# Performance work log

Measured on AMD Instinct MI355X. Metric: run time of the kernel, lower is better.

## Reference

```python
import jax, jax.numpy as jnp
import numpy as np

# Model dims (match init_kwargs)
B, S, H = 1, 2048, 1024
E = 16            # n_routed_experts
I = 768           # moe_intermediate_size
TOPK = 4          # num_experts_per_tok
G = 4             # n_group
TOPK_G = 2        # topk_group
SCALE = 2.5       # routed_scaling_factor
N_SHARED = 1      # n_shared_experts


def setup_inputs() -> dict:
    key = jax.random.key(0)
    ks = jax.random.split(key, 9)
    def rn(k, shape, scale=0.02):
        return jax.random.normal(k, shape, dtype=jnp.float32) * scale
    return dict(
        hidden_states=jax.random.normal(ks[0], (B, S, H), dtype=jnp.float32),
        gate_w=rn(ks[1], (E, H)),
        gate_bias=jax.random.normal(ks[2], (E,), dtype=jnp.float32) * 0.1,
        w1=rn(ks[3], (E, I, H)),   # gate_proj weights [out,in]
        w2=rn(ks[4], (E, H, I)),   # down_proj weights
        w3=rn(ks[5], (E, I, H)),   # up_proj weights
        ws1=rn(ks[6], (I * N_SHARED, H)),
        ws2=rn(ks[7], (H, I * N_SHARED)),
        ws3=rn(ks[8], (I * N_SHARED, H)),
    )


def _route(x, gate_w, gate_bias):
    """noaux_tc routing: sigmoid scores + bias, group top-k, top_k experts."""
    n = x.shape[0]
    logits = jnp.einsum('nh,eh->ne', x.astype(jnp.float32), gate_w)  # [N,E]
    scores = jax.nn.sigmoid(logits)
    sb = scores + gate_bias                                          # biased scores
    # group score = sum of top-2 biased scores in each group
    gs = sb.reshape(n, G, E // G)
    group_scores = jnp.sum(jax.lax.top_k(gs, 2)[0], axis=-1)         # [N,G]
    _, gidx = jax.lax.top_k(group_scores, TOPK_G)                    # [N,TOPK_G]
    gmask = jnp.sum(jax.nn.one_hot(gidx, G, dtype=sb.dtype), axis=1) # [N,G]
    emask = jnp.repeat(gmask, E // G, axis=-1)                       # [N,E]
    masked = jnp.where(emask > 0, sb, -jnp.inf)
    _, tidx = jax.lax.top_k(masked, TOPK)                            # [N,TOPK]
    w = jnp.take_along_axis(scores, tidx, axis=1)                    # unbiased weights
    w = w / (jnp.sum(w, axis=-1, keepdims=True) + 1e-20)             # norm_topk_prob
    return tidx, w * SCALE


def reference(hidden_states, gate_w, gate_bias, w1, w2, w3, ws1, ws2, ws3):
    b, s, h = hidden_states.shape
    x = hidden_states.reshape(-1, h)                                 # [N,H]
    tidx, tw = _route(x, gate_w, gate_bias)
    n = x.shape[0]
    # dense combine weights [N,E] (zero for unselected experts)
    combine = jnp.zeros((n, E), x.dtype).at[jnp.arange(n)[:, None], tidx].add(tw)
    # grouped SwiGLU experts (dense-over-experts reference form)
    g = jnp.einsum('nh,eih->nei', x, w1)
    u = jnp.einsum('nh,eih->nei', x, w3)
    hact = jax.nn.silu(g) * u * combine[:, :, None]
    y = jnp.einsum('nei,ehi->nh', hact, w2)
    # shared expert SwiGLU
    shared = jnp.einsum('ni,hi->nh', jax.nn.silu(x @ ws1.T) * (x @ ws3.T), ws2)
    return (y + shared).reshape(b, s, h)
```

## Files before the change

### kernel.cpp

```cpp
#include <hip/hip_runtime.h>
#include <hip/hip_bf16.h>
#include <math.h>

#define N_TOK 2048
#define H_DIM 1024
#define N_EXP 16
#define I_DIM 768
#define TOPK 4
#define SCALE 2.5f

#define GU_SLOTS 256
#define DN_SLOTS 192
#define GU_TAB (8 * GU_SLOTS)
#define DN_TAB (8 * DN_SLOTS)
#define GU_NY (I_DIM / 64)
#define DN_NY (H_DIM / 128)
#define MAX_GRP 832

typedef __attribute__((ext_vector_type(8))) short bf16x8;
typedef __attribute__((ext_vector_type(4))) float f32x4;

#define OFF_COUNTS   0
#define OFF_OFFSETS  128
#define OFF_WGU      256
#define OFF_WDN      (OFF_WGU + GU_TAB*4)
#define OFF_TOKIDS   (OFF_WDN + DN_TAB*4)
#define OFF_TOKW     (OFF_TOKIDS + N_EXP*N_TOK*4)
#define OFF_XB       (OFF_TOKW + N_EXP*N_TOK*4)
#define OFF_HACT     (OFF_XB + (size_t)N_TOK*H_DIM*2)
#define OFF_GWT      (OFF_HACT + (size_t)N_TOK*(TOPK+1)*I_DIM*2)

__device__ __forceinline__ ushort f2bf(float f) {
    union { __hip_bfloat16 h; ushort u; } cv;
    cv.h = __float2bfloat16(f);
    return cv.u;
}
__device__ __forceinline__ unsigned pack2(float lo, float hi) {
    return (unsigned)f2bf(lo) | ((unsigned)f2bf(hi) << 16);
}
__device__ __forceinline__ void async_copy16(const void* g, void* l) {
    __builtin_amdgcn_global_load_lds(
        (const __attribute__((address_space(1))) unsigned int*)g,
        (__attribute__((address_space(3))) unsigned int*)l, 16, 0, 0);
}

__global__ void k_gwt(const float* __restrict__ gw, float* __restrict__ gwT) {
    int i = blockIdx.x * 256 + threadIdx.x;
    int k = i >> 4, e = i & 15;
    gwT[i] = gw[e * H_DIM + k];
}

__launch_bounds__(256)
__global__ void k_route(const float* __restrict__ x, const float* __restrict__ gwT,
                        const float* __restrict__ gb,
                        int* __restrict__ counts, int* __restrict__ tok_ids,
                        float* __restrict__ tok_w, ushort* __restrict__ xb) {
    __shared__ float lgs[4][N_EXP + 1];
    int tid = threadIdx.x;
    int wv = tid >> 6, lane = tid & 63;
    int e = lane & 15, ks = lane >> 4;
    int n = blockIdx.x * 4 + wv;

    const float* xr = x + (size_t)n * H_DIM + ks * 256;
    ushort* xbr = xb + (size_t)n * H_DIM + ks * 256;
    const float* wr = gwT + ks * 256 * N_EXP + e;
    float a0 = 0.f, a1 = 0.f, a2 = 0.f, a3 = 0.f;
#pragma unroll 8
    for (int k = 0; k < 256; k += 4) {
        float4 xv = *(const float4*)(xr + k);
        a0 += xv.x * wr[(k + 0) * N_EXP];
        a1 += xv.y * wr[(k + 1) * N_EXP];
        a2 += xv.z * wr[(k + 2) * N_EXP];
        a3 += xv.w * wr[(k + 3) * N_EXP];
        if (e == 0) {
            uint2 p;
            p.x = pack2(xv.x, xv.y);
            p.y = pack2(xv.z, xv.w);
            *(uint2*)(xbr + k) = p;
        }
    }
    float acc = (a0 + a1) + (a2 + a3);
    acc += __shfl_xor(acc, 16);
    acc += __shfl_xor(acc, 32);
    if (lane < 16) lgs[wv][lane] = acc;
    __syncthreads();

    if (tid < 4) {
        int n2 = blockIdx.x * 4 + tid;
        float sc[N_EXP], sb[N_EXP];
        for (int ee = 0; ee < N_EXP; ee++) {
            float l = lgs[tid][ee];
            sc[ee] = 1.f / (1.f + expf(-l));
            sb[ee] = sc[ee] + gb[ee];
        }
        float gsc[4];
        for (int g = 0; g < 4; g++) {
            float m1 = -1e30f, m2 = -1e30f;
            for (int j = 0; j < 4; j++) {
                float v = sb[4 * g + j];
                if (v > m1) { m2 = m1; m1 = v; }
                else if (v > m2) m2 = v;
            }
            gsc[g] = m1 + m2;
        }
        int g1 = 0;
        for (int g = 1; g < 4; g++) if (gsc[g] > gsc[g1]) g1 = g;
        int g2 = -1;
        for (int g = 0; g < 4; g++) {
            if (g == g1) continue;
            if (g2 < 0 || gsc[g] > gsc[g2]) g2 = g;
        }
        bool allowed[N_EXP];
        for (int ee = 0; ee < N_EXP; ee++) {
            int grp = ee >> 2;
            allowed[ee] = (grp == g1) || (grp == g2);
        }
        int chosen[TOPK];
        float wsum = 0.f;
        for (int k = 0; k < TOPK; k++) {
            int best = -1;
            for (int ee = 0; ee < N_EXP; ee++) {
                if (!allowed[ee]) continue;
                if (best < 0 || sb[ee] > sb[best]) best = ee;
            }
            chosen[k] = best;
            allowed[best] = false;
            wsum += sc[best];
        }
        float inv = SCALE / (wsum + 1e-20f);
        for (int k = 0; k < TOPK; k++) {
            int ee = chosen[k];
            int p = atomicAdd(&counts[ee], 1);
            tok_ids[ee * N_TOK + p] = n2;
            tok_w[ee * N_TOK + p] = sc[ee] * inv;
        }
    }
}

__global__ void k_scan(const int* __restrict__ counts, int* __restrict__ offsets,
                       int* __restrict__ wgu, int* __restrict__ wdn) {
    __shared__ int nmt_s[20], gpe_s[20];
    __shared__ int geb[20], deb[20];
    __shared__ int gmeta[MAX_GRP];
    __shared__ int gslot[MAX_GRP];
    __shared__ int ngu_s, ntot_s;
    int tid = threadIdx.x;
    for (int i = tid; i < GU_TAB; i += 256) wgu[i] = -1;
    for (int i = tid; i < DN_TAB; i += 256) wdn[i] = -1;
    if (tid < 17) {
        int c = (tid == 16) ? N_TOK : counts[tid];
        int nm = (c + 127) >> 7;
        nmt_s[tid] = nm;
        gpe_s[tid] = (nm + 3) >> 2;
    }
    __syncthreads();
    if (tid == 0) {
        int off = 0;
        for (int e = 0; e < N_EXP; e++) { offsets[e] = off; off += counts[e]; }
        offsets[N_EXP] = off;
        int g = 0, d = 0;
        for (int e = 0; e <= N_EXP; e++) {
            geb[e] = g; g += GU_NY * gpe_s[e];
            deb[e] = d; d += DN_NY * gpe_s[e];
        }
        geb[N_EXP + 1] = g; deb[N_EXP + 1] = d;
        ngu_s = g; ntot_s = g + d;
    }
    __syncthreads();
    int ngu = ngu_s, ntot = ntot_s;
    for (int g = tid; g < ntot; g += 256) {
        bool gu = g < ngu;
        int r = gu ? g : g - ngu;
        const int* eb = gu ? geb : deb;
        int e = 0;
        while (eb[e + 1] <= r) e++;
        int rem = r - eb[e];
        int gp = gpe_s[e];
        int y = rem / gp, mc = rem - y * gp;
        int m0t = mc * 4;
        int size = nmt_s[e] - m0t; if (size > 4) size = 4;
        gmeta[g] = e | (m0t << 5) | (y << 9) | (size << 24);
    }
    __syncthreads();
    if (tid < 8) {
        int s = 0;
        for (int g = tid; g < ngu; g += 8) { gslot[g] = s; s += (gmeta[g] >> 24); }
    } else if (tid < 16) {
        int c = tid - 8, s = 0;
        for (int g = ngu + c; g < ntot; g += 8) { gslot[g] = s; s += (gmeta[g] >> 24); }
    }
    __syncthreads();
    int k = tid & 3;
    for (int g = tid >> 2; g < ntot; g += 64) {
        int p = gmeta[g];
        int size = (p >> 24);
        if (k >= size) continue;
        int desc = (p & 0x1FFF) + (k << 5);
        bool gu = g < ngu;
        int r = gu ? g : g - ngu;
        int idx = (r & 7) + 8 * (gslot[g] + k);
        if (gu) wgu[idx] = desc; else wdn[idx] = desc;
    }
}

__launch_bounds__(256, 3)
__global__ void k_gateup(const ushort* __restrict__ xb, const float* __restrict__ w1,
                         const float* __restrict__ w3, const float* __restrict__ ws1,
                         const float* __restrict__ ws3, const int* __restrict__ counts,
                         const int* __restrict__ offsets, const int* __restrict__ wgu,
                         const int* __restrict__ tok_ids, const float* __restrict__ tok_w,
                         ushort* __restrict__ hact) {
    int desc = wgu[blockIdx.x];
    if (desc < 0) return;
    int e = desc & 31;
    int m0 = ((desc >> 5) & 15) * 128;
    int i0 = ((desc >> 9) & 15) * 64;
    int Me = (e == N_EXP) ? N_TOK : counts[e];
    const float* W1 = (e == N_EXP) ? ws1 : w1 + (size_t)e * I_DIM * H_DIM;
    const float* W3 = (e == N_EXP) ? ws3 : w3 + (size_t)e * I_DIM * H_DIM;
    int base = offsets[e];

    __shared__ ushort As[128][64];
    __shared__ ushort Bs[128][64];
    __shared__ float tws[128];

    int tid = threadIdx.x;
    int wv = tid >> 6, lane = tid & 63;
    int seg = lane & 7, rsub = lane >> 3;
    int gch = (seg ^ rsub) * 8;

    if (tid < 128) {
        int r = m0 + tid;
        tws[tid] = (e == N_EXP) ? 1.f : ((r < Me) ? tok_w[e * N_TOK + r] : 0.f);
    }

    const ushort* aptr[4];
#pragma unroll
    for (int j = 0; j < 4; j++) {
        int gr = m0 + wv * 32 + j * 8 + rsub;
        int tok = (e == N_EXP) ? gr : ((gr < Me) ? tok_ids[e * N_TOK + gr] : 0);
        aptr[j] = xb + (size_t)tok * H_DIM + gch;
    }
    const float* bptrf[4];
#pragma unroll
    for (int j = 0; j < 4; j++) {
        int r = wv * 32 + j * 8 + rsub;
        const float* W = (r < 64) ? (W1 + (size_t)(i0 + r) * H_DIM)
                                  : (W3 + (size_t)(i0 + r - 64) * H_DIM);
        bptrf[j] = W + gch;
    }

    int quad = lane >> 4, lr = lane & 15, rx = lr & 7;
    f32x4 acc[2][8] = {};

    const int NK = H_DIM / 64;
    float4 bv0[4], bv1[4];
#pragma unroll
    for (int j = 0; j < 4; j++) {
        bv0[j] = *(const float4*)(bptrf[j]);
        bv1[j] = *(const float4*)(bptrf[j] + 4);
    }
    for (int k = 0; k < NK; k++) {
        int off = k * 64;
#pragma unroll
        for (int j = 0; j < 4; j++) async_copy16(aptr[j] + off, &As[wv * 32 + j * 8][0]);
#pragma unroll
        for (int j = 0; j < 4; j++) {
            uint4 p;
            p.x = pack2(bv0[j].x, bv0[j].y);
            p.y = pack2(bv0[j].z, bv0[j].w);
            p.z = pack2(bv1[j].x, bv1[j].y);
            p.w = pack2(bv1[j].z, bv1[j].w);
            *(uint4*)&Bs[wv * 32 + j * 8 + rsub][seg * 8] = p;
        }
        if (k + 1 < NK) {
#pragma unroll
            for (int j = 0; j < 4; j++) {
                bv0[j] = *(const float4*)(bptrf[j] + off + 64);
                bv1[j] = *(const float4*)(bptrf[j] + off + 68);
            }
        }
        __syncthreads();
#pragma unroll
        for (int ks = 0; ks < 2; ks++) {
            int co = ((ks * 4 + quad) ^ rx) * 8;
            bf16x8 a0 = *(const bf16x8*)&As[wv * 32 + lr][co];
            bf16x8 a1 = *(const bf16x8*)&As[wv * 32 + 16 + lr][co];
#pragma unroll
            for (int ni = 0; ni < 8; ni++) {
                bf16x8 bf = *(const bf16x8*)&Bs[ni * 16 + lr][co];
                acc[0][ni] = __builtin_amdgcn_mfma_f32_16x16x32_bf16(a0, bf, acc[0][ni], 0, 0, 0);
                acc[1][ni] = __builtin_amdgcn_mfma_f32_16x16x32_bf16(a1, bf, acc[1][ni], 0, 0, 0);
            }
        }
        __syncthreads();
    }

#pragma unroll
    for (int mi = 0; mi < 2; mi++) {
#pragma unroll
        for (int ni = 0; ni < 4; ni++) {
            f32x4 g = acc[mi][ni];
            f32x4 u = acc[mi][ni + 4];
#pragma unroll
            for (int rg = 0; rg < 4; rg++) {
                int ml = wv * 32 + mi * 16 + quad * 4 + rg;
                int row = m0 + ml;
                if (row < Me) {
                    float gg = g[rg], uu = u[rg];
                    float act = (gg / (1.f + expf(-gg))) * uu * tws[ml];
                    hact[(size_t)(base + row) * I_DIM + i0 + ni * 16 + lr] = f2bf(act);
                }
            }
        }
    }
}

__launch_bounds__(256, 3)
__global__ void k_down(const ushort* __restrict__ hact, const float* __restrict__ w2,
                       const float* __restrict__ ws2, const int* __restrict__ counts,
                       const int* __restrict__ offsets, const int* __restrict__ wdn,
                       const int* __restrict__ tok_ids, float* __restrict__ out) {
    int desc = wdn[blockIdx.x];
    if (desc < 0) return;
    int e = desc & 31;
    int m0 = ((desc >> 5) & 15) * 128;
    int h0 = ((desc >> 9) & 15) * 128;
    int Me = (e == N_EXP) ? N_TOK : counts[e];
    const float* W2 = (e == N_EXP) ? ws2 : w2 + (size_t)e * H_DIM * I_DIM;
    int base = offsets[e];

    __shared__ ushort As[128][64];
    __shared__ ushort Bs[128][64];
    __shared__ int toks[128];

    int tid = threadIdx.x;
    int wv = tid >> 6, lane = tid & 63;
    int seg = lane & 7, rsub = lane >> 3;
    int gch = (seg ^ rsub) * 8;

    if (tid < 128) {
        int r = m0 + tid;
        toks[tid] = (e == N_EXP) ? r : ((r < Me) ? tok_ids[e * N_TOK + r] : 0);
    }

    const ushort* aptr[4];
#pragma unroll
    for (int j = 0; j < 4; j++) {
        int row = wv * 32 + j * 8 + rsub;
        aptr[j] = hact + (size_t)(base + m0 + row) * I_DIM + gch;
    }
    const float* bptrf[4];
#pragma unroll
    for (int j = 0; j < 4; j++) {
        int r = wv * 32 + j * 8 + rsub;
        bptrf[j] = W2 + (size_t)(h0 + r) * I_DIM + gch;
    }

    int quad = lane >> 4, lr = lane & 15, rx = lr & 7;
    f32x4 acc[2][8] = {};

    const int NK = I_DIM / 64;
    float4 bv0[4], bv1[4];
#pragma unroll
    for (int j = 0; j < 4; j++) {
        bv0[j] = *(const float4*)(bptrf[j]);
        bv1[j] = *(const float4*)(bptrf[j] + 4);
    }
    for (int k = 0; k < NK; k++) {
        int off = k * 64;
#pragma unroll
        for (int j = 0; j < 4; j++) async_copy16(aptr[j] + off, &As[wv * 32 + j * 8][0]);
#pragma unroll
        for (int j = 0; j < 4; j++) {
            uint4 p;
            p.x = pack2(bv0[j].x, bv0[j].y);
            p.y = pack2(bv0[j].z, bv0[j].w);
            p.z = pack2(bv1[j].x, bv1[j].y);
            p.w = pack2(bv1[j].z, bv1[j].w);
            *(uint4*)&Bs[wv * 32 + j * 8 + rsub][seg * 8] = p;
        }
        if (k + 1 < NK) {
#pragma unroll
            for (int j = 0; j < 4; j++) {
                bv0[j] = *(const float4*)(bptrf[j] + off + 64);
                bv1[j] = *(const float4*)(bptrf[j] + off + 68);
            }
        }
        __syncthreads();
#pragma unroll
        for (int ks = 0; ks < 2; ks++) {
            int co = ((ks * 4 + quad) ^ rx) * 8;
            bf16x8 a0 = *(const bf16x8*)&As[wv * 32 + lr][co];
            bf16x8 a1 = *(const bf16x8*)&As[wv * 32 + 16 + lr][co];
#pragma unroll
            for (int ni = 0; ni < 8; ni++) {
                bf16x8 bf = *(const bf16x8*)&Bs[ni * 16 + lr][co];
                acc[0][ni] = __builtin_amdgcn_mfma_f32_16x16x32_bf16(a0, bf, acc[0][ni], 0, 0, 0);
                acc[1][ni] = __builtin_amdgcn_mfma_f32_16x16x32_bf16(a1, bf, acc[1][ni], 0, 0, 0);
            }
        }
        __syncthreads();
    }

#pragma unroll
    for (int mi = 0; mi < 2; mi++) {
#pragma unroll
        for (int ni = 0; ni < 8; ni++) {
#pragma unroll
            for (int rg = 0; rg < 4; rg++) {
                int ml = wv * 32 + mi * 16 + quad * 4 + rg;
                int row = m0 + ml;
                if (row < Me) {
                    int tok = toks[ml];
                    atomicAdd(&out[(size_t)tok * H_DIM + h0 + ni * 16 + lr],
                              acc[mi][ni][rg]);
                }
            }
        }
    }
}

extern "C" void kernel_launch(void* const* d_in, const int* in_sizes, int n_in,
                              void* d_out, int out_size, void* d_ws, size_t ws_size,
                              hipStream_t stream) {
    const float* x   = (const float*)d_in[0];
    const float* gw  = (const float*)d_in[1];
    const float* gb  = (const float*)d_in[2];
    const float* w1  = (const float*)d_in[3];
    const float* w2  = (const float*)d_in[4];
    const float* w3  = (const float*)d_in[5];
    const float* ws1 = (const float*)d_in[6];
    const float* ws2 = (const float*)d_in[7];
    const float* ws3 = (const float*)d_in[8];
    float* out = (float*)d_out;

    char* wsb = (char*)d_ws;
    int* counts   = (int*)(wsb + OFF_COUNTS);
    int* offsets  = (int*)(wsb + OFF_OFFSETS);
    int* wgu      = (int*)(wsb + OFF_WGU);
    int* wdn      = (int*)(wsb + OFF_WDN);
    int* tok_ids  = (int*)(wsb + OFF_TOKIDS);
    float* tok_w  = (float*)(wsb + OFF_TOKW);
    ushort* xb    = (ushort*)(wsb + OFF_XB);
    ushort* hact  = (ushort*)(wsb + OFF_HACT);
    float* gwT    = (float*)(wsb + OFF_GWT);

    hipMemsetAsync(wsb, 0, 128, stream);
    hipMemsetAsync(d_out, 0, (size_t)out_size * 4, stream);

    k_gwt<<<N_EXP * H_DIM / 256, 256, 0, stream>>>(gw, gwT);
    k_route<<<N_TOK / 4, 256, 0, stream>>>(x, gwT, gb, counts, tok_ids, tok_w, xb);
    k_scan<<<1, 256, 0, stream>>>(counts, offsets, wgu, wdn);
    k_gateup<<<GU_TAB, 256, 0, stream>>>(xb, w1, w3, ws1, ws3, counts, offsets,
                                         wgu, tok_ids, tok_w, hact);
    k_down<<<DN_TAB, 256, 0, stream>>>(hact, w2, ws2, counts, offsets, wdn,
                                       tok_ids, out);
}
```

Measured before the change: 364.7 us.

## Replace atomic scatter in down projection with staged buffer and per-token reduce

The down-projection kernel now writes each expert's partial outputs to a dense per-slot temporary buffer instead of issuing fp32 atomicAdds into the output. Routing records an inverse map from each token's top-k choices to expert slots, and a new reduce kernel sums the shared-expert row and the four routed rows per token. The output memset is dropped. This removes atomic contention and scattered atomic traffic, at the cost of an extra kernel launch and roughly 40MB of temporary writes and reads.

```diff
diff --git a/kernel.cpp b/kernel.cpp
--- a/kernel.cpp
+++ b/kernel.cpp
@@ -26,9 +26,11 @@
 #define OFF_WDN      (OFF_WGU + GU_TAB*4)
 #define OFF_TOKIDS   (OFF_WDN + DN_TAB*4)
 #define OFF_TOKW     (OFF_TOKIDS + N_EXP*N_TOK*4)
-#define OFF_XB       (OFF_TOKW + N_EXP*N_TOK*4)
+#define OFF_INV      (OFF_TOKW + N_EXP*N_TOK*4)
+#define OFF_XB       (OFF_INV + N_TOK*TOPK*4)
 #define OFF_HACT     (OFF_XB + (size_t)N_TOK*H_DIM*2)
 #define OFF_GWT      (OFF_HACT + (size_t)N_TOK*(TOPK+1)*I_DIM*2)
+#define OFF_YTMP     (OFF_GWT + N_EXP*H_DIM*4)
 
 __device__ __forceinline__ ushort f2bf(float f) {
     union { __hip_bfloat16 h; ushort u; } cv;
@@ -54,7 +56,8 @@
 __global__ void k_route(const float* __restrict__ x, const float* __restrict__ gwT,
                         const float* __restrict__ gb,
                         int* __restrict__ counts, int* __restrict__ tok_ids,
-                        float* __restrict__ tok_w, ushort* __restrict__ xb) {
+                        float* __restrict__ tok_w, ushort* __restrict__ xb,
+                        int* __restrict__ inv) {
     __shared__ float lgs[4][N_EXP + 1];
     int tid = threadIdx.x;
     int wv = tid >> 6, lane = tid & 63;
@@ -127,12 +130,13 @@
             allowed[best] = false;
             wsum += sc[best];
         }
-        float inv = SCALE / (wsum + 1e-20f);
+        float inv_w = SCALE / (wsum + 1e-20f);
         for (int k = 0; k < TOPK; k++) {
             int ee = chosen[k];
             int p = atomicAdd(&counts[ee], 1);
             tok_ids[ee * N_TOK + p] = n2;
-            tok_w[ee * N_TOK + p] = sc[ee] * inv;
+            tok_w[ee * N_TOK + p] = sc[ee] * inv_w;
+            inv[n2 * TOPK + k] = (ee << 16) | p;
         }
     }
 }
@@ -320,7 +324,7 @@
 __global__ void k_down(const ushort* __restrict__ hact, const float* __restrict__ w2,
                        const float* __restrict__ ws2, const int* __restrict__ counts,
                        const int* __restrict__ offsets, const int* __restrict__ wdn,
-                       const int* __restrict__ tok_ids, float* __restrict__ out) {
+                       float* __restrict__ ytmp) {
     int desc = wdn[blockIdx.x];
     if (desc < 0) return;
     int e = desc & 31;
@@ -332,17 +336,11 @@
 
     __shared__ ushort As[128][64];
     __shared__ ushort Bs[128][64];
-    __shared__ int toks[128];
 
     int tid = threadIdx.x;
     int wv = tid >> 6, lane = tid & 63;
     int seg = lane & 7, rsub = lane >> 3;
     int gch = (seg ^ rsub) * 8;
-
-    if (tid < 128) {
-        int r = m0 + tid;
-        toks[tid] = (e == N_EXP) ? r : ((r < Me) ? tok_ids[e * N_TOK + r] : 0);
-    }
 
     const ushort* aptr[4];
 #pragma unroll
@@ -412,13 +410,28 @@
                 int ml = wv * 32 + mi * 16 + quad * 4 + rg;
                 int row = m0 + ml;
                 if (row < Me) {
-                    int tok = toks[ml];
-                    atomicAdd(&out[(size_t)tok * H_DIM + h0 + ni * 16 + lr],
-                              acc[mi][ni][rg]);
+                    ytmp[(size_t)(base + row) * H_DIM + h0 + ni * 16 + lr] =
+                        acc[mi][ni][rg];
                 }
             }
         }
     }
+}
+
+__launch_bounds__(256)
+__global__ void k_reduce(const float* __restrict__ ytmp, const int* __restrict__ inv,
+                         const int* __restrict__ offsets, float* __restrict__ out) {
+    int t = blockIdx.x, tid = threadIdx.x;
+    const float4* yt = (const float4*)ytmp;
+    float4 s = yt[(size_t)(offsets[N_EXP] + t) * (H_DIM / 4) + tid];
+#pragma unroll
+    for (int k = 0; k < TOPK; k++) {
+        int v = inv[t * TOPK + k];
+        int slot = offsets[v >> 16] + (v & 0xFFFF);
+        float4 a = yt[(size_t)slot * (H_DIM / 4) + tid];
+        s.x += a.x; s.y += a.y; s.z += a.z; s.w += a.w;
+    }
+    ((float4*)out)[(size_t)t * (H_DIM / 4) + tid] = s;
 }
 
 extern "C" void kernel_launch(void* const* d_in, const int* in_sizes, int n_in,
@@ -442,18 +455,19 @@
     int* wdn      = (int*)(wsb + OFF_WDN);
     int* tok_ids  = (int*)(wsb + OFF_TOKIDS);
     float* tok_w  = (float*)(wsb + OFF_TOKW);
+    int* inv      = (int*)(wsb + OFF_INV);
     ushort* xb    = (ushort*)(wsb + OFF_XB);
     ushort* hact  = (ushort*)(wsb + OFF_HACT);
     float* gwT    = (float*)(wsb + OFF_GWT);
+    float* ytmp   = (float*)(wsb + OFF_YTMP);
 
     hipMemsetAsync(wsb, 0, 128, stream);
-    hipMemsetAsync(d_out, 0, (size_t)out_size * 4, stream);
 
     k_gwt<<<N_EXP * H_DIM / 256, 256, 0, stream>>>(gw, gwT);
-    k_route<<<N_TOK / 4, 256, 0, stream>>>(x, gwT, gb, counts, tok_ids, tok_w, xb);
+    k_route<<<N_TOK / 4, 256, 0, stream>>>(x, gwT, gb, counts, tok_ids, tok_w, xb, inv);
     k_scan<<<1, 256, 0, stream>>>(counts, offsets, wgu, wdn);
     k_gateup<<<GU_TAB, 256, 0, stream>>>(xb, w1, w3, ws1, ws3, counts, offsets,
                                          wgu, tok_ids, tok_w, hact);
-    k_down<<<DN_TAB, 256, 0, stream>>>(hact, w2, ws2, counts, offsets, wdn,
-                                       tok_ids, out);
-}
+    k_down<<<DN_TAB, 256, 0, stream>>>(hact, w2, ws2, counts, offsets, wdn, ytmp);
+    k_reduce<<<N_TOK, 256, 0, stream>>>(ytmp, inv, offsets, out);
+}
```

Result: faster. 351.4 us, median of 2 (-3.6%).
